# Kernel tuning notes

Hardware: AMD Instinct MI355X
Metric: run time of the kernel (lower is better)

## Reference

```python
import jax, jax.numpy as jnp
import numpy as np
from math import lgamma

B = 8
RES = 64
RES_OUT = 32
L_IN = RES // 2 - 1        # 31
L_OUT = RES_OUT // 2 - 1   # 15
SPINS_IN = (0, 1)
SPINS_OUT = (0, 1, 2)
C_IN = 64
C_OUT = 128
K_IN = (L_IN + 1) ** 2     # 1024 coefficients, ordered by (ell, m): idx = ell^2 + (m + ell)
K_OUT = (L_OUT + 1) ** 2   # 256
EPS_BN = 1e-5
EPS_NL = 1e-6


def _wigner_d_col(l, s, thetas):
    """Wigner small-d column d^l_{m,-s}(theta) for m in [-l, l]; (2l+1, n_theta)."""
    n = -s
    out = np.zeros((2 * l + 1, thetas.size))
    if l < abs(s):
        return out
    cb = np.cos(thetas / 2.0)
    sb = np.sin(thetas / 2.0)
    for mi, m in enumerate(range(-l, l + 1)):
        pref = 0.5 * (lgamma(l + m + 1) + lgamma(l - m + 1)
                      + lgamma(l + n + 1) + lgamma(l - n + 1))
        acc = np.zeros_like(thetas)
        for k in range(max(0, n - m), min(l + n, l - m) + 1):
            lg = pref - (lgamma(l + n - k + 1) + lgamma(k + 1)
                         + lgamma(m - n + k + 1) + lgamma(l - m - k + 1))
            acc += ((-1.0) ** (m - n + k)) * np.exp(lg) \
                   * cb ** (2 * l + n - m - 2 * k) * sb ** (m - n + 2 * k)
        out[mi] = acc
    return out


def _sylm_grid(spin, ell_max, res):
    """Spin-weighted spherical harmonics sampled on equiangular grid: (K, res, res)."""
    thetas = (np.arange(res) + 0.5) * np.pi / res
    phis = np.arange(res) * 2.0 * np.pi / res
    Y = np.zeros(((ell_max + 1) ** 2, res, res), dtype=np.complex64)
    phase = np.exp(1j * np.outer(np.arange(-ell_max, ell_max + 1), phis))
    for l in range(ell_max + 1):
        d = _wigner_d_col(l, spin, thetas)               # (2l+1, res)
        norm = np.sqrt((2 * l + 1) / (4.0 * np.pi))
        for mi, m in enumerate(range(-l, l + 1)):
            Y[l * l + mi] = (((-1.0) ** m) * norm * d[mi][:, None]
                             * phase[m + ell_max][None, :])
    return Y


# Deterministic transform constants (computed once at import).
_THETA = (np.arange(RES) + 0.5) * np.pi / RES
_QUAD_W = (np.sin(_THETA) * (np.pi / RES) * (2.0 * np.pi / RES)).astype(np.float32)
Y_IN = np.stack([_sylm_grid(s, L_IN, RES) for s in SPINS_IN])          # (Si,K_IN,RES,RES)
Y_IN_W = (np.conj(Y_IN) * _QUAD_W[None, None, :, None]).astype(np.complex64)
Y_OUT = np.stack([_sylm_grid(s, L_OUT, RES_OUT) for s in SPINS_OUT])   # (So,K_OUT,32,32)
ELL_OUT = np.floor(np.sqrt(np.arange(K_OUT))).astype(np.int32)         # degree of each coeff


def setup_inputs() -> dict:
    key = jax.random.key(0)
    ks = jax.random.split(key, 8)
    shape_x = (B, RES, RES, len(SPINS_IN), C_IN)
    kern_shape = (L_IN + 1, len(SPINS_IN), len(SPINS_OUT), C_IN, C_OUT)
    scale = 1.0 / np.sqrt(len(SPINS_IN) * C_IN)
    return {
        "x_real": jax.random.normal(ks[0], shape_x, jnp.float32),
        "x_imag": jax.random.normal(ks[1], shape_x, jnp.float32),
        "kernel_real": jax.random.normal(ks[2], kern_shape, jnp.float32) * scale,
        "kernel_imag": jax.random.normal(ks[3], kern_shape, jnp.float32) * scale,
        "gamma": jax.random.uniform(ks[4], (len(SPINS_OUT), C_OUT), jnp.float32, 0.5, 1.5),
        "beta_real": jax.random.normal(ks[5], (len(SPINS_OUT), C_OUT), jnp.float32) * 0.1,
        "beta_imag": jax.random.normal(ks[6], (len(SPINS_OUT), C_OUT), jnp.float32) * 0.1,
        "nonlin_bias": jax.random.normal(ks[7], (len(SPINS_OUT), C_OUT), jnp.float32) * 0.1,
    }


def _forward(x_real, x_imag, kernel_real, kernel_imag, gamma,
             beta_real, beta_imag, nonlin_bias):
    x = x_real + 1j * x_imag                                   # (B,RES,RES,Si,Ci)
    # Forward spin-weighted spherical harmonic transform, per input spin.
    coeffs = jnp.einsum('btpiu,iktp->bkiu', x, jnp.asarray(Y_IN_W))  # (B,K_IN,Si,Ci)
    # Spectral pooling: keep degrees ell <= L_OUT (coeffs ordered by ell).
    coeffs = coeffs[:, :K_OUT]
    # Per-degree spectral convolution mixing spins and channels.
    kernel = (kernel_real + 1j * kernel_imag)[jnp.asarray(ELL_OUT)]  # (K_OUT,Si,So,Ci,Co)
    out_coeffs = jnp.einsum('bkiu,kisud->bksd', coeffs, kernel)      # (B,K_OUT,So,Co)
    # Inverse transform on the downsampled grid, per output spin.
    fmap = jnp.einsum('bksd,sktp->btpsd', out_coeffs, jnp.asarray(Y_OUT))
    # Equivariant batch norm: mean subtraction only for spin 0 channels.
    spin0 = (jnp.asarray(np.array(SPINS_OUT)) == 0)[:, None]         # (So,1)
    mean = jnp.mean(fmap, axis=(0, 1, 2)) * spin0                    # (So,Co)
    centered = fmap - mean
    var = jnp.mean(jnp.abs(centered) ** 2, axis=(0, 1, 2))           # (So,Co)
    beta = (beta_real + 1j * beta_imag) * spin0
    y = centered * (gamma / jnp.sqrt(var + EPS_BN)) + beta
    # Magnitude nonlinearity: y * relu(|y| + b) / (|y| + eps).
    mag = jnp.abs(y)
    return y * (jax.nn.relu(mag + nonlin_bias) / (mag + EPS_NL))


def reference(x_real, x_imag, kernel_real, kernel_imag, gamma,
              beta_real, beta_imag, nonlin_bias):
    return _forward(x_real, x_imag, kernel_real, kernel_imag, gamma,
                    beta_real, beta_imag, nonlin_bias)
```

## Files before the change

### kernel.cpp

```cpp
#include <hip/hip_runtime.h>
#include <hip/hip_fp16.h>
#include <math.h>


#define PI_D 3.14159265358979323846

#define OFF_A_IN    ((size_t)24320)
#define OFF_A_OUT   ((size_t)155648)
#define OFF_STATS   ((size_t)254208)
#define OFF_R1      ((size_t)260608)
#define OFF_R2      ((size_t)25426688)
#define OFF_W       ((size_t)67108864)

__constant__ double LF[31] = {
    0.0, 0.0, 0.6931471805599453, 1.791759469228055, 3.1780538303479458,
    4.787491742782046, 6.579251212010101, 8.525161361065415,
    10.604602902745251, 12.801827480081469, 15.104412573075516,
    17.502307845873887, 19.987214495661885, 22.552163853123425,
    25.19122118273868, 27.89927138384089, 30.671860106080672,
    33.50507345013689, 36.39544520803305, 39.339884187199495,
    42.335616460753485, 45.38013889847691, 48.47118135183523,
    51.60667556776438, 54.78472939811232, 58.00360522298052,
    61.261701761002, 64.55753862700634, 67.88974313718154,
    71.25703896716801, 74.65823634883016};

__device__ inline int isqrt_k(int k) {
    int l = (int)sqrtf((float)k + 0.5f);
    while (l * l > k) --l;
    while ((l + 1) * (l + 1) <= k) ++l;
    return l;
}

__device__ double wigner_d_rec(int l, int m, int n, double theta) {
    int an = n < 0 ? -n : n;
    int am = m < 0 ? -m : m;
    if (l < an || l < am) return 0.0;
    int kmin = max(0, n - m), kmax = min(l + n, l - m);
    if (kmax < kmin) return 0.0;
    double cb = cos(0.5 * theta), sb = sin(0.5 * theta);
    double pref = 0.5 * (LF[l + m] + LF[l - m] + LF[l + n] + LF[l - n]);
    double lterm = pref
        - (LF[l + n - kmin] + LF[kmin] + LF[m - n + kmin] + LF[l - m - kmin])
        + (double)(2 * l + n - m - 2 * kmin) * log(cb)
        + (double)(m - n + 2 * kmin) * log(sb);
    double term = exp(lterm);
    if ((m - n + kmin) & 1) term = -term;
    double r = (sb * sb) / (cb * cb);
    double acc = term;
    for (int k = kmin; k < kmax; ++k) {
        term *= -((double)((l + n - k) * (l - m - k)) * r)
                / ((double)((k + 1) * (m - n + k + 1)));
        acc += term;
    }
    return acc;
}

__global__ __launch_bounds__(512, 2) void k_phi_tables(const float* __restrict__ xr,
                                                       const float* __restrict__ xi,
                                                       __half2* __restrict__ F,
                                                       float* __restrict__ A_in,
                                                       float* __restrict__ A_out,
                                                       float* __restrict__ stats,
                                                       const float* __restrict__ kr,
                                                       const float* __restrict__ ki,
                                                       float4* __restrict__ W) {
    if (blockIdx.x >= 512) {
        if (blockIdx.x >= 627) {
            int e0 = (blockIdx.x - 627) * 512 + threadIdx.x;
            const float2* kr2 = (const float2*)kr;
            const float2* ki2 = (const float2*)ki;
#pragma unroll
            for (int j = 0; j < 16; ++j) {
                int e = e0 + j * 24576;
                int dp = e & 63, r = e >> 6;
                float2 a = kr2[(size_t)r * 64 + dp];
                float2 b = ki2[(size_t)r * 64 + dp];
                W[e] = make_float4(a.x, a.y, b.x, b.y);
            }
            return;
        }
        int idx = (blockIdx.x - 512) * 512 + threadIdx.x;
        if (idx < 32768) {
            int t = idx & 63, k = (idx >> 6) & 255, i = idx >> 14;
            int l = isqrt_k(k);
            int m = k - l * l - l;
            double theta = ((double)t + 0.5) * PI_D / 64.0;
            double w = sin(theta) * (PI_D / 64.0) * (2.0 * PI_D / 64.0);
            double norm = sqrt((2.0 * l + 1.0) / (4.0 * PI_D));
            double d = wigner_d_rec(l, m, -i, theta);
            A_in[idx] = (float)(((m & 1) ? -1.0 : 1.0) * norm * w * d);
            return;
        }
        idx -= 32768;
        if (idx < 24576) {
            int t = idx & 31, k = (idx >> 5) & 255, s = idx >> 13;
            int l = isqrt_k(k);
            int m = k - l * l - l;
            double theta = ((double)t + 0.5) * PI_D / 32.0;
            double norm = sqrt((2.0 * l + 1.0) / (4.0 * PI_D));
            double d = wigner_d_rec(l, m, -s, theta);
            A_out[idx] = (float)(((m & 1) ? -1.0 : 1.0) * norm * d);
            return;
        }
        idx -= 24576;
        if (idx < 1152) stats[idx] = 0.f;
        return;
    }
    int bt = blockIdx.x;
    int iu = threadIdx.x & 127, mh = threadIdx.x >> 7;
    int mi0 = mh * 8;
    float2 acc[8], w[8], st[8];
#pragma unroll
    for (int j = 0; j < 8; ++j) {
        int m = mi0 + j - 15;
        float sy, sx;
        __sincosf(-(float)m * (float)(PI_D / 32.0), &sy, &sx);
        st[j] = make_float2(sx, sy);
        w[j] = make_float2(1.f, 0.f);
        acc[j] = make_float2(0.f, 0.f);
    }
    const float* xrb = xr + (size_t)bt * 8192 + iu;
    const float* xib = xi + (size_t)bt * 8192 + iu;
    for (int p = 0; p < 32; ++p) {
        float a  = xrb[(size_t)p * 128];
        float b  = xib[(size_t)p * 128];
        float a2 = xrb[(size_t)(p + 32) * 128];
        float b2 = xib[(size_t)(p + 32) * 128];
        float sar = a + a2, sai = b + b2;
        float dar = a - a2, dai = b - b2;
#pragma unroll
        for (int j = 0; j < 8; ++j) {
            float ur = (j & 1) ? sar : dar;
            float ui = (j & 1) ? sai : dai;
            acc[j].x += ur * w[j].x - ui * w[j].y;
            acc[j].y += ur * w[j].y + ui * w[j].x;
            float nx = w[j].x * st[j].x - w[j].y * st[j].y;
            w[j].y = w[j].x * st[j].y + w[j].y * st[j].x;
            w[j].x = nx;
        }
    }
    __half2* Fb = F + (size_t)bt * 31 * 128 + iu;
#pragma unroll
    for (int j = 0; j < 8; ++j) {
        int mi = mi0 + j;
        if (mi < 31) Fb[(size_t)mi * 128] = __float22half2_rn(acc[j]);
    }
}

__global__ __launch_bounds__(256, 4) void k_theta_in(const __half2* __restrict__ F,
                                                     const float* __restrict__ A_in,
                                                     __half2* __restrict__ coeffs) {
    __shared__ float A[16][64];
    __shared__ float2 red[2][16][64];
    int mi = blockIdx.x, b = blockIdx.y, z = blockIdx.z;
    int m = mi - 15;
    int am = m < 0 ? -m : m;
    int tid = threadIdx.x;
    for (int idx = tid; idx < 1024; idx += 256) {
        int j = idx >> 6, t = idx & 63;
        float v = 0.f;
        if (j >= am) v = A_in[((size_t)z * 256 + (j * j + j + m)) * 64 + t];
        A[j][t] = v;
    }
    __syncthreads();
    int iu_l = tid & 63, th = tid >> 6;
    int iu = z * 64 + iu_l;
    float2 acc[16];
#pragma unroll
    for (int j = 0; j < 16; ++j) acc[j] = make_float2(0.f, 0.f);
    const __half2* Fb = F + ((size_t)b * 64 * 31 + mi) * 128 + iu;
    for (int tt = 0; tt < 16; ++tt) {
        int t = th * 16 + tt;
        float2 f = __half22float2(Fb[(size_t)t * 31 * 128]);
#pragma unroll
        for (int j = 0; j < 16; ++j) {
            float a = A[j][t];
            acc[j].x += a * f.x;
            acc[j].y += a * f.y;
        }
    }
    if (th >= 2) {
#pragma unroll
        for (int j = 0; j < 16; ++j) red[th - 2][j][iu_l] = acc[j];
    }
    __syncthreads();
    if (th < 2) {
#pragma unroll
        for (int j = 0; j < 16; ++j) {
            float2 r = red[th][j][iu_l];
            acc[j].x += r.x;
            acc[j].y += r.y;
        }
    }
    __syncthreads();
    if (th == 1) {
#pragma unroll
        for (int j = 0; j < 16; ++j) red[0][j][iu_l] = acc[j];
    }
    __syncthreads();
    if (th == 0) {
#pragma unroll
        for (int j = 0; j < 16; ++j) {
            if (j >= am) {
                float2 r = red[0][j][iu_l];
                coeffs[((size_t)b * 256 + (j * j + j + m)) * 128 + iu] =
                    __float22half2_rn(make_float2(acc[j].x + r.x, acc[j].y + r.y));
            }
        }
    }
}

__global__ __launch_bounds__(192, 2) void k_mix(const __half2* __restrict__ coeffs,
                                                const float4* __restrict__ W,
                                                __half2* __restrict__ oc) {
    __shared__ float2 cs[4][128];
    int bx = blockIdx.x;
    int k = ((bx & 7) << 5) + (bx >> 3);
    int b0 = blockIdx.y * 4;
    int tid = threadIdx.x;
    for (int idx = tid; idx < 512; idx += 192) {
        int bb = idx >> 7, iu = idx & 127;
        cs[bb][iu] =
            __half22float2(coeffs[((size_t)(b0 + bb) * 256 + k) * 128 + iu]);
    }
    __syncthreads();
    int s = tid >> 6, dp = tid & 63;
    int l = isqrt_k(k);
    float2 acc[4][2];
#pragma unroll
    for (int bb = 0; bb < 4; ++bb) {
        acc[bb][0] = make_float2(0.f, 0.f);
        acc[bb][1] = make_float2(0.f, 0.f);
    }
    const float4* W0 = W + (size_t)(6 * l + s) * 4096 + dp;
    const float4* W1 = W0 + (size_t)3 * 4096;
    float4 cur[4];
#pragma unroll
    for (int j = 0; j < 4; ++j) cur[j] = W0[(size_t)j * 64];
    for (int g = 0; g < 32; ++g) {
        float4 nxt[4];
        if (g < 31) {
            int iu0 = (g + 1) * 4;
            const float4* P = (iu0 < 64) ? (W0 + (size_t)iu0 * 64)
                                         : (W1 + (size_t)(iu0 - 64) * 64);
#pragma unroll
            for (int j = 0; j < 4; ++j) nxt[j] = P[(size_t)j * 64];
        }
#pragma unroll
        for (int j = 0; j < 4; ++j) {
            int iu = g * 4 + j;
            float2 wr = make_float2(cur[j].x, cur[j].y);
            float2 wi = make_float2(cur[j].z, cur[j].w);
#pragma unroll
            for (int bb = 0; bb < 4; ++bb) {
                float2 cv = cs[bb][iu];
                acc[bb][0].x += cv.x * wr.x - cv.y * wi.x;
                acc[bb][0].y += cv.x * wi.x + cv.y * wr.x;
                acc[bb][1].x += cv.x * wr.y - cv.y * wi.y;
                acc[bb][1].y += cv.x * wi.y + cv.y * wr.y;
            }
        }
        if (g < 31) {
#pragma unroll
            for (int j = 0; j < 4; ++j) cur[j] = nxt[j];
        }
    }
#pragma unroll
    for (int bb = 0; bb < 4; ++bb) {
        size_t o = ((size_t)(b0 + bb) * 256 + k) * 384 + s * 128 + 2 * dp;
        oc[o]     = __float22half2_rn(acc[bb][0]);
        oc[o + 1] = __float22half2_rn(acc[bb][1]);
    }
}

__global__ __launch_bounds__(192, 4) void k_theta_out(const __half2* __restrict__ oc,
                                                      const float* __restrict__ A_out,
                                                      __half2* __restrict__ G,
                                                      float* __restrict__ ssr,
                                                      float* __restrict__ ssi,
                                                      float* __restrict__ ssq) {
    __shared__ float Ao[3][16][32];
    int mi = blockIdx.x, b = blockIdx.y, z = blockIdx.z;
    int m = mi - 15;
    int am = m < 0 ? -m : m;
    int tid = threadIdx.x;
    for (int idx = tid; idx < 1536; idx += 192) {
        int s = idx >> 9, j = (idx >> 5) & 15, t = idx & 31;
        float v = 0.f;
        if (j >= am) v = A_out[((size_t)s * 256 + (j * j + j + m)) * 32 + t];
        Ao[s][j][t] = v;
    }
    __syncthreads();
    int sd = z * 192 + tid;
    int s = sd >> 7;
    float2 c[16];
#pragma unroll
    for (int j = 0; j < 16; ++j) {
        c[j] = make_float2(0.f, 0.f);
        if (j >= am)
            c[j] = __half22float2(oc[((size_t)b * 256 + (j * j + j + m)) * 384 + sd]);
    }
    float sq = 0.f, sr = 0.f, si = 0.f;
    for (int t = 0; t < 32; ++t) {
        float fr = 0.f, fi = 0.f;
#pragma unroll
        for (int j = 0; j < 16; ++j) {
            float a = Ao[s][j][t];
            fr += a * c[j].x;
            fi += a * c[j].y;
        }
        G[(((size_t)b * 32 + t) * 31 + mi) * 384 + sd] =
            __float22half2_rn(make_float2(fr, fi));
        sq += fr * fr + fi * fi;
        if (mi == 15) { sr += fr; si += fi; }
    }
    atomicAdd(&ssq[sd], sq);
    if (mi == 15) {
        atomicAdd(&ssr[sd], sr);
        atomicAdd(&ssi[sd], si);
    }
}

__global__ __launch_bounds__(192, 2) void k_synth_final(const __half2* __restrict__ G,
                                                        const float* __restrict__ ssr,
                                                        const float* __restrict__ ssi,
                                                        const float* __restrict__ ssq,
                                                        const float* __restrict__ gamma,
                                                        const float* __restrict__ betar,
                                                        const float* __restrict__ betai,
                                                        const float* __restrict__ bias,
                                                        float* __restrict__ out) {
    int bt = blockIdx.x;
    int sd = blockIdx.y * 192 + threadIdx.x;
    int s = sd >> 7;
    float2 g[31], st[31];
#pragma unroll
    for (int mi = 0; mi < 31; ++mi) {
        g[mi] = __half22float2(G[((size_t)bt * 31 + mi) * 384 + sd]);
        float sy, sx;
        __sincosf((float)(mi - 15) * (float)(PI_D / 16.0), &sy, &sx);
        st[mi] = make_float2(sx, sy);
    }
    const float invN = 1.0f / 256.0f;
    float mur = 0.f, mui = 0.f;
    if (s == 0) { mur = ssr[sd] * invN; mui = ssi[sd] * invN; }
    float var = ssq[sd] * invN - (mur * mur + mui * mui);
    float scale = gamma[sd] / sqrtf(var + 1e-5f);
    float br = (s == 0) ? betar[sd] : 0.f;
    float bi = (s == 0) ? betai[sd] : 0.f;
    float bb = bias[sd];
    float* ob = out + (size_t)bt * 32 * 384 + sd;
    for (int p = 0; p < 16; ++p) {
        float fr = 0.f, fi = 0.f, fr2 = 0.f, fi2 = 0.f;
#pragma unroll
        for (int mi = 0; mi < 31; ++mi) {
            fr += g[mi].x;
            fi += g[mi].y;
            if (mi & 1) { fr2 += g[mi].x; fi2 += g[mi].y; }
            else        { fr2 -= g[mi].x; fi2 -= g[mi].y; }
        }
        {
            float yr = (fr - mur) * scale + br;
            float yi = (fi - mui) * scale + bi;
            float mag = sqrtf(yr * yr + yi * yi);
            float f = fmaxf(mag + bb, 0.f) / (mag + 1e-6f);
            ob[(size_t)p * 384] = yr * f;
        }
        {
            float yr = (fr2 - mur) * scale + br;
            float yi = (fi2 - mui) * scale + bi;
            float mag = sqrtf(yr * yr + yi * yi);
            float f = fmaxf(mag + bb, 0.f) / (mag + 1e-6f);
            ob[(size_t)(p + 16) * 384] = yr * f;
        }
#pragma unroll
        for (int mi = 0; mi < 31; ++mi) {
            float nx = g[mi].x * st[mi].x - g[mi].y * st[mi].y;
            g[mi].y = g[mi].x * st[mi].y + g[mi].y * st[mi].x;
            g[mi].x = nx;
        }
    }
}

extern "C" void kernel_launch(void* const* d_in, const int* in_sizes, int n_in,
                              void* d_out, int out_size, void* d_ws, size_t ws_size,
                              hipStream_t stream) {
    const float* xr    = (const float*)d_in[0];
    const float* xi    = (const float*)d_in[1];
    const float* kr    = (const float*)d_in[2];
    const float* ki    = (const float*)d_in[3];
    const float* gamma = (const float*)d_in[4];
    const float* betar = (const float*)d_in[5];
    const float* betai = (const float*)d_in[6];
    const float* bias  = (const float*)d_in[7];
    float* out = (float*)d_out;

    char* ws = (char*)d_ws;
    float*   A_in   = (float*)(ws + OFF_A_IN);
    float*   A_out  = (float*)(ws + OFF_A_OUT);
    float*   stats  = (float*)(ws + OFF_STATS);
    float*   ssr    = stats;
    float*   ssi    = stats + 384;
    float*   ssq    = stats + 768;
    __half2* F      = (__half2*)(ws + OFF_R1);
    __half2* oc     = (__half2*)(ws + OFF_R1);
    __half2* coeffs = (__half2*)(ws + OFF_R2);
    __half2* G      = (__half2*)(ws + OFF_R2);
    float4*  W      = (float4*)(ws + OFF_W);

    k_phi_tables<<<675, 512, 0, stream>>>(xr, xi, F, A_in, A_out, stats, kr, ki, W);
    k_theta_in<<<dim3(31, 8, 2), 256, 0, stream>>>(F, A_in, coeffs);
    k_mix<<<dim3(256, 2), 192, 0, stream>>>(coeffs, W, oc);
    k_theta_out<<<dim3(31, 8, 2), 192, 0, stream>>>(oc, A_out, G, ssr, ssi, ssq);
    k_synth_final<<<dim3(256, 2), 192, 0, stream>>>(G, ssr, ssi, ssq,
                                                    gamma, betar, betai, bias, out);
}
```

Baseline: 179.5 us.

## Fuse five stage kernels into one persistent kernel with grid barriers

Replaces the five separate launches with a single persistent 256-block kernel that runs every stage in turn. Stages are separated by software grid barriers built on an atomic counter, and each block processes two logical blocks per stage. The aim is to remove launch and drain gaps between stages. In exchange, occupancy drops to one block per CU, the barriers cost spin-waits, and the barrier has a timeout that could silently break correctness, plus an extra memset.

Result: slower. 330.6 us (+84.2%).

```diff
diff --git a/kernel.cpp b/kernel.cpp
--- a/kernel.cpp
+++ b/kernel.cpp
@@ -8,6 +8,7 @@
 #define OFF_A_IN    ((size_t)24320)
 #define OFF_A_OUT   ((size_t)155648)
 #define OFF_STATS   ((size_t)254208)
+#define OFF_BAR     ((size_t)259072)
 #define OFF_R1      ((size_t)260608)
 #define OFF_R2      ((size_t)25426688)
 #define OFF_W       ((size_t)67108864)
@@ -55,32 +56,60 @@
     return acc;
 }
 
-__global__ __launch_bounds__(512, 2) void k_phi_tables(const float* __restrict__ xr,
-                                                       const float* __restrict__ xi,
-                                                       __half2* __restrict__ F,
-                                                       float* __restrict__ A_in,
-                                                       float* __restrict__ A_out,
-                                                       float* __restrict__ stats,
-                                                       const float* __restrict__ kr,
-                                                       const float* __restrict__ ki,
-                                                       float4* __restrict__ W) {
-    if (blockIdx.x >= 512) {
-        if (blockIdx.x >= 627) {
-            int e0 = (blockIdx.x - 627) * 512 + threadIdx.x;
-            const float2* kr2 = (const float2*)kr;
-            const float2* ki2 = (const float2*)ki;
-#pragma unroll
-            for (int j = 0; j < 16; ++j) {
-                int e = e0 + j * 24576;
-                int dp = e & 63, r = e >> 6;
-                float2 a = kr2[(size_t)r * 64 + dp];
-                float2 b = ki2[(size_t)r * 64 + dp];
-                W[e] = make_float4(a.x, a.y, b.x, b.y);
-            }
-            return;
-        }
-        int idx = (blockIdx.x - 512) * 512 + threadIdx.x;
-        if (idx < 32768) {
+__device__ __forceinline__ void gbar(unsigned* bar, unsigned target) {
+    __syncthreads();
+    if (threadIdx.x == 0) {
+        __threadfence();
+        __hip_atomic_fetch_add(bar, 1u, __ATOMIC_RELEASE,
+                               __HIP_MEMORY_SCOPE_AGENT);
+        unsigned tries = 0;
+        while (__hip_atomic_load(bar, __ATOMIC_ACQUIRE,
+                                 __HIP_MEMORY_SCOPE_AGENT) < target) {
+            __builtin_amdgcn_s_sleep(2);
+            if (++tries > 200000u) break;
+        }
+        __threadfence();
+    }
+    __syncthreads();
+}
+
+__global__ __launch_bounds__(256, 1) void k_mega(
+    const float* __restrict__ xr, const float* __restrict__ xi,
+    const float* __restrict__ kr, const float* __restrict__ ki,
+    const float* __restrict__ gamma, const float* __restrict__ betar,
+    const float* __restrict__ betai, const float* __restrict__ bias,
+    float* __restrict__ out,
+    float* __restrict__ A_in, float* __restrict__ A_out,
+    float* __restrict__ stats,
+    __half2* __restrict__ F, __half2* __restrict__ coeffs,
+    __half2* __restrict__ oc, __half2* __restrict__ G,
+    float4* __restrict__ W, unsigned* __restrict__ bar) {
+    __shared__ union {
+        struct { float A[16][64]; float2 red[2][16][64]; } p2;
+        struct { float2 cs[4][128]; } p3;
+        struct { float Ao[3][16][32]; } p4;
+    } sm;
+
+    float* ssr = stats;
+    float* ssi = stats + 384;
+    float* ssq = stats + 768;
+
+    int bid = blockIdx.x, tid = threadIdx.x;
+    int gidx = bid * 256 + tid;
+
+    {
+        const float2* kr2 = (const float2*)kr;
+        const float2* ki2 = (const float2*)ki;
+#pragma unroll
+        for (int j = 0; j < 6; ++j) {
+            int e = gidx + j * 65536;
+            int dp = e & 63, r = e >> 6;
+            float2 a = kr2[(size_t)r * 64 + dp];
+            float2 b = ki2[(size_t)r * 64 + dp];
+            W[e] = make_float4(a.x, a.y, b.x, b.y);
+        }
+        if (gidx < 32768) {
+            int idx = gidx;
             int t = idx & 63, k = (idx >> 6) & 255, i = idx >> 14;
             int l = isqrt_k(k);
             int m = k - l * l - l;
@@ -89,10 +118,8 @@
             double norm = sqrt((2.0 * l + 1.0) / (4.0 * PI_D));
             double d = wigner_d_rec(l, m, -i, theta);
             A_in[idx] = (float)(((m & 1) ? -1.0 : 1.0) * norm * w * d);
-            return;
-        }
-        idx -= 32768;
-        if (idx < 24576) {
+        } else if (gidx < 57344) {
+            int idx = gidx - 32768;
             int t = idx & 31, k = (idx >> 5) & 255, s = idx >> 13;
             int l = isqrt_k(k);
             int m = k - l * l - l;
@@ -100,284 +127,287 @@
             double norm = sqrt((2.0 * l + 1.0) / (4.0 * PI_D));
             double d = wigner_d_rec(l, m, -s, theta);
             A_out[idx] = (float)(((m & 1) ? -1.0 : 1.0) * norm * d);
-            return;
-        }
-        idx -= 24576;
-        if (idx < 1152) stats[idx] = 0.f;
-        return;
-    }
-    int bt = blockIdx.x;
-    int iu = threadIdx.x & 127, mh = threadIdx.x >> 7;
-    int mi0 = mh * 8;
-    float2 acc[8], w[8], st[8];
-#pragma unroll
-    for (int j = 0; j < 8; ++j) {
-        int m = mi0 + j - 15;
-        float sy, sx;
-        __sincosf(-(float)m * (float)(PI_D / 32.0), &sy, &sx);
-        st[j] = make_float2(sx, sy);
-        w[j] = make_float2(1.f, 0.f);
-        acc[j] = make_float2(0.f, 0.f);
-    }
-    const float* xrb = xr + (size_t)bt * 8192 + iu;
-    const float* xib = xi + (size_t)bt * 8192 + iu;
-    for (int p = 0; p < 32; ++p) {
-        float a  = xrb[(size_t)p * 128];
-        float b  = xib[(size_t)p * 128];
-        float a2 = xrb[(size_t)(p + 32) * 128];
-        float b2 = xib[(size_t)(p + 32) * 128];
-        float sar = a + a2, sai = b + b2;
-        float dar = a - a2, dai = b - b2;
-#pragma unroll
-        for (int j = 0; j < 8; ++j) {
-            float ur = (j & 1) ? sar : dar;
-            float ui = (j & 1) ? sai : dai;
-            acc[j].x += ur * w[j].x - ui * w[j].y;
-            acc[j].y += ur * w[j].y + ui * w[j].x;
-            float nx = w[j].x * st[j].x - w[j].y * st[j].y;
-            w[j].y = w[j].x * st[j].y + w[j].y * st[j].x;
-            w[j].x = nx;
-        }
-    }
-    __half2* Fb = F + (size_t)bt * 31 * 128 + iu;
-#pragma unroll
-    for (int j = 0; j < 8; ++j) {
-        int mi = mi0 + j;
-        if (mi < 31) Fb[(size_t)mi * 128] = __float22half2_rn(acc[j]);
-    }
-}
-
-__global__ __launch_bounds__(256, 4) void k_theta_in(const __half2* __restrict__ F,
-                                                     const float* __restrict__ A_in,
-                                                     __half2* __restrict__ coeffs) {
-    __shared__ float A[16][64];
-    __shared__ float2 red[2][16][64];
-    int mi = blockIdx.x, b = blockIdx.y, z = blockIdx.z;
-    int m = mi - 15;
-    int am = m < 0 ? -m : m;
-    int tid = threadIdx.x;
-    for (int idx = tid; idx < 1024; idx += 256) {
-        int j = idx >> 6, t = idx & 63;
-        float v = 0.f;
-        if (j >= am) v = A_in[((size_t)z * 256 + (j * j + j + m)) * 64 + t];
-        A[j][t] = v;
-    }
-    __syncthreads();
-    int iu_l = tid & 63, th = tid >> 6;
-    int iu = z * 64 + iu_l;
-    float2 acc[16];
-#pragma unroll
-    for (int j = 0; j < 16; ++j) acc[j] = make_float2(0.f, 0.f);
-    const __half2* Fb = F + ((size_t)b * 64 * 31 + mi) * 128 + iu;
-    for (int tt = 0; tt < 16; ++tt) {
-        int t = th * 16 + tt;
-        float2 f = __half22float2(Fb[(size_t)t * 31 * 128]);
+        } else if (gidx < 58496) {
+            stats[gidx - 57344] = 0.f;
+        }
+    }
+    for (int rr = 0; rr < 2; ++rr) {
+        int bt = bid + 256 * rr;
+        int iu = tid & 127, mh2 = tid >> 7;
+        float2 acc[16], w[16], st[16];
 #pragma unroll
         for (int j = 0; j < 16; ++j) {
-            float a = A[j][t];
-            acc[j].x += a * f.x;
-            acc[j].y += a * f.y;
-        }
-    }
-    if (th >= 2) {
-#pragma unroll
-        for (int j = 0; j < 16; ++j) red[th - 2][j][iu_l] = acc[j];
-    }
-    __syncthreads();
-    if (th < 2) {
+            int m = mh2 * 16 + j - 15;
+            float sy, sx;
+            __sincosf(-(float)m * (float)(PI_D / 32.0), &sy, &sx);
+            st[j] = make_float2(sx, sy);
+            w[j] = make_float2(1.f, 0.f);
+            acc[j] = make_float2(0.f, 0.f);
+        }
+        const float* xrb = xr + (size_t)bt * 8192 + iu;
+        const float* xib = xi + (size_t)bt * 8192 + iu;
+        for (int p = 0; p < 32; ++p) {
+            float a  = xrb[(size_t)p * 128];
+            float b  = xib[(size_t)p * 128];
+            float a2 = xrb[(size_t)(p + 32) * 128];
+            float b2 = xib[(size_t)(p + 32) * 128];
+            float sar = a + a2, sai = b + b2;
+            float dar = a - a2, dai = b - b2;
+#pragma unroll
+            for (int j = 0; j < 16; ++j) {
+                float ur = (j & 1) ? sar : dar;
+                float ui = (j & 1) ? sai : dai;
+                acc[j].x += ur * w[j].x - ui * w[j].y;
+                acc[j].y += ur * w[j].y + ui * w[j].x;
+                float nx = w[j].x * st[j].x - w[j].y * st[j].y;
+                w[j].y = w[j].x * st[j].y + w[j].y * st[j].x;
+                w[j].x = nx;
+            }
+        }
+        __half2* Fb = F + (size_t)bt * 31 * 128 + iu;
 #pragma unroll
         for (int j = 0; j < 16; ++j) {
-            float2 r = red[th][j][iu_l];
-            acc[j].x += r.x;
-            acc[j].y += r.y;
-        }
-    }
-    __syncthreads();
-    if (th == 1) {
-#pragma unroll
-        for (int j = 0; j < 16; ++j) red[0][j][iu_l] = acc[j];
-    }
-    __syncthreads();
-    if (th == 0) {
-#pragma unroll
-        for (int j = 0; j < 16; ++j) {
-            if (j >= am) {
-                float2 r = red[0][j][iu_l];
-                coeffs[((size_t)b * 256 + (j * j + j + m)) * 128 + iu] =
-                    __float22half2_rn(make_float2(acc[j].x + r.x, acc[j].y + r.y));
-            }
-        }
-    }
-}
-
-__global__ __launch_bounds__(192, 2) void k_mix(const __half2* __restrict__ coeffs,
-                                                const float4* __restrict__ W,
-                                                __half2* __restrict__ oc) {
-    __shared__ float2 cs[4][128];
-    int bx = blockIdx.x;
-    int k = ((bx & 7) << 5) + (bx >> 3);
-    int b0 = blockIdx.y * 4;
-    int tid = threadIdx.x;
-    for (int idx = tid; idx < 512; idx += 192) {
-        int bb = idx >> 7, iu = idx & 127;
-        cs[bb][iu] =
-            __half22float2(coeffs[((size_t)(b0 + bb) * 256 + k) * 128 + iu]);
-    }
-    __syncthreads();
-    int s = tid >> 6, dp = tid & 63;
-    int l = isqrt_k(k);
-    float2 acc[4][2];
-#pragma unroll
-    for (int bb = 0; bb < 4; ++bb) {
-        acc[bb][0] = make_float2(0.f, 0.f);
-        acc[bb][1] = make_float2(0.f, 0.f);
-    }
-    const float4* W0 = W + (size_t)(6 * l + s) * 4096 + dp;
-    const float4* W1 = W0 + (size_t)3 * 4096;
-    float4 cur[4];
-#pragma unroll
-    for (int j = 0; j < 4; ++j) cur[j] = W0[(size_t)j * 64];
-    for (int g = 0; g < 32; ++g) {
-        float4 nxt[4];
-        if (g < 31) {
-            int iu0 = (g + 1) * 4;
-            const float4* P = (iu0 < 64) ? (W0 + (size_t)iu0 * 64)
-                                         : (W1 + (size_t)(iu0 - 64) * 64);
-#pragma unroll
-            for (int j = 0; j < 4; ++j) nxt[j] = P[(size_t)j * 64];
-        }
-#pragma unroll
-        for (int j = 0; j < 4; ++j) {
-            int iu = g * 4 + j;
-            float2 wr = make_float2(cur[j].x, cur[j].y);
-            float2 wi = make_float2(cur[j].z, cur[j].w);
+            int mi = mh2 * 16 + j;
+            if (mi < 31) Fb[(size_t)mi * 128] = __float22half2_rn(acc[j]);
+        }
+    }
+    gbar(bar, 256);
+
+    for (int rr = 0; rr < 2; ++rr) {
+        int lb = bid + 256 * rr;
+        if (lb < 496) {
+            int mi = lb % 31;
+            int q = lb / 31;
+            int b = q >> 1, z = q & 1;
+            int m = mi - 15;
+            int am = m < 0 ? -m : m;
+            for (int idx = tid; idx < 1024; idx += 256) {
+                int j = idx >> 6, t = idx & 63;
+                float v = 0.f;
+                if (j >= am) v = A_in[((size_t)z * 256 + (j * j + j + m)) * 64 + t];
+                sm.p2.A[j][t] = v;
+            }
+            __syncthreads();
+            int iu_l = tid & 63, th = tid >> 6;
+            int iu = z * 64 + iu_l;
+            float2 acc[16];
+#pragma unroll
+            for (int j = 0; j < 16; ++j) acc[j] = make_float2(0.f, 0.f);
+            const __half2* Fb = F + ((size_t)b * 64 * 31 + mi) * 128 + iu;
+            for (int tt = 0; tt < 16; ++tt) {
+                int t = th * 16 + tt;
+                float2 f = __half22float2(Fb[(size_t)t * 31 * 128]);
+#pragma unroll
+                for (int j = 0; j < 16; ++j) {
+                    float a = sm.p2.A[j][t];
+                    acc[j].x += a * f.x;
+                    acc[j].y += a * f.y;
+                }
+            }
+            if (th >= 2) {
+#pragma unroll
+                for (int j = 0; j < 16; ++j) sm.p2.red[th - 2][j][iu_l] = acc[j];
+            }
+            __syncthreads();
+            if (th < 2) {
+#pragma unroll
+                for (int j = 0; j < 16; ++j) {
+                    float2 r = sm.p2.red[th][j][iu_l];
+                    acc[j].x += r.x;
+                    acc[j].y += r.y;
+                }
+            }
+            __syncthreads();
+            if (th == 1) {
+#pragma unroll
+                for (int j = 0; j < 16; ++j) sm.p2.red[0][j][iu_l] = acc[j];
+            }
+            __syncthreads();
+            if (th == 0) {
+#pragma unroll
+                for (int j = 0; j < 16; ++j) {
+                    if (j >= am) {
+                        float2 r = sm.p2.red[0][j][iu_l];
+                        coeffs[((size_t)b * 256 + (j * j + j + m)) * 128 + iu] =
+                            __float22half2_rn(
+                                make_float2(acc[j].x + r.x, acc[j].y + r.y));
+                    }
+                }
+            }
+        }
+        __syncthreads();
+    }
+    gbar(bar, 512);
+
+    for (int rr = 0; rr < 2; ++rr) {
+        int lb = bid + 256 * rr;
+        int y = lb >> 8;
+        int bxk = lb & 255;
+        int k = ((bxk & 7) << 5) + (bxk >> 3);
+        int b0 = y * 4;
+        for (int idx = tid; idx < 512; idx += 256) {
+            int bb = idx >> 7, iuu = idx & 127;
+            sm.p3.cs[bb][iuu] =
+                __half22float2(coeffs[((size_t)(b0 + bb) * 256 + k) * 128 + iuu]);
+        }
+        __syncthreads();
+        if (tid < 192) {
+            int s = tid >> 6, dp = tid & 63;
+            int l = isqrt_k(k);
+            float2 acc[4][2];
 #pragma unroll
             for (int bb = 0; bb < 4; ++bb) {
-                float2 cv = cs[bb][iu];
-                acc[bb][0].x += cv.x * wr.x - cv.y * wi.x;
-                acc[bb][0].y += cv.x * wi.x + cv.y * wr.x;
-                acc[bb][1].x += cv.x * wr.y - cv.y * wi.y;
-                acc[bb][1].y += cv.x * wi.y + cv.y * wr.y;
-            }
-        }
-        if (g < 31) {
-#pragma unroll
-            for (int j = 0; j < 4; ++j) cur[j] = nxt[j];
-        }
-    }
-#pragma unroll
-    for (int bb = 0; bb < 4; ++bb) {
-        size_t o = ((size_t)(b0 + bb) * 256 + k) * 384 + s * 128 + 2 * dp;
-        oc[o]     = __float22half2_rn(acc[bb][0]);
-        oc[o + 1] = __float22half2_rn(acc[bb][1]);
-    }
-}
-
-__global__ __launch_bounds__(192, 4) void k_theta_out(const __half2* __restrict__ oc,
-                                                      const float* __restrict__ A_out,
-                                                      __half2* __restrict__ G,
-                                                      float* __restrict__ ssr,
-                                                      float* __restrict__ ssi,
-                                                      float* __restrict__ ssq) {
-    __shared__ float Ao[3][16][32];
-    int mi = blockIdx.x, b = blockIdx.y, z = blockIdx.z;
-    int m = mi - 15;
-    int am = m < 0 ? -m : m;
-    int tid = threadIdx.x;
-    for (int idx = tid; idx < 1536; idx += 192) {
-        int s = idx >> 9, j = (idx >> 5) & 15, t = idx & 31;
-        float v = 0.f;
-        if (j >= am) v = A_out[((size_t)s * 256 + (j * j + j + m)) * 32 + t];
-        Ao[s][j][t] = v;
-    }
-    __syncthreads();
-    int sd = z * 192 + tid;
-    int s = sd >> 7;
-    float2 c[16];
-#pragma unroll
-    for (int j = 0; j < 16; ++j) {
-        c[j] = make_float2(0.f, 0.f);
-        if (j >= am)
-            c[j] = __half22float2(oc[((size_t)b * 256 + (j * j + j + m)) * 384 + sd]);
-    }
-    float sq = 0.f, sr = 0.f, si = 0.f;
-    for (int t = 0; t < 32; ++t) {
-        float fr = 0.f, fi = 0.f;
-#pragma unroll
-        for (int j = 0; j < 16; ++j) {
-            float a = Ao[s][j][t];
-            fr += a * c[j].x;
-            fi += a * c[j].y;
-        }
-        G[(((size_t)b * 32 + t) * 31 + mi) * 384 + sd] =
-            __float22half2_rn(make_float2(fr, fi));
-        sq += fr * fr + fi * fi;
-        if (mi == 15) { sr += fr; si += fi; }
-    }
-    atomicAdd(&ssq[sd], sq);
-    if (mi == 15) {
-        atomicAdd(&ssr[sd], sr);
-        atomicAdd(&ssi[sd], si);
-    }
-}
-
-__global__ __launch_bounds__(192, 2) void k_synth_final(const __half2* __restrict__ G,
-                                                        const float* __restrict__ ssr,
-                                                        const float* __restrict__ ssi,
-                                                        const float* __restrict__ ssq,
-                                                        const float* __restrict__ gamma,
-                                                        const float* __restrict__ betar,
-                                                        const float* __restrict__ betai,
-                                                        const float* __restrict__ bias,
-                                                        float* __restrict__ out) {
-    int bt = blockIdx.x;
-    int sd = blockIdx.y * 192 + threadIdx.x;
-    int s = sd >> 7;
-    float2 g[31], st[31];
-#pragma unroll
-    for (int mi = 0; mi < 31; ++mi) {
-        g[mi] = __half22float2(G[((size_t)bt * 31 + mi) * 384 + sd]);
-        float sy, sx;
-        __sincosf((float)(mi - 15) * (float)(PI_D / 16.0), &sy, &sx);
-        st[mi] = make_float2(sx, sy);
-    }
-    const float invN = 1.0f / 256.0f;
-    float mur = 0.f, mui = 0.f;
-    if (s == 0) { mur = ssr[sd] * invN; mui = ssi[sd] * invN; }
-    float var = ssq[sd] * invN - (mur * mur + mui * mui);
-    float scale = gamma[sd] / sqrtf(var + 1e-5f);
-    float br = (s == 0) ? betar[sd] : 0.f;
-    float bi = (s == 0) ? betai[sd] : 0.f;
-    float bb = bias[sd];
-    float* ob = out + (size_t)bt * 32 * 384 + sd;
-    for (int p = 0; p < 16; ++p) {
-        float fr = 0.f, fi = 0.f, fr2 = 0.f, fi2 = 0.f;
-#pragma unroll
-        for (int mi = 0; mi < 31; ++mi) {
-            fr += g[mi].x;
-            fi += g[mi].y;
-            if (mi & 1) { fr2 += g[mi].x; fi2 += g[mi].y; }
-            else        { fr2 -= g[mi].x; fi2 -= g[mi].y; }
-        }
-        {
-            float yr = (fr - mur) * scale + br;
-            float yi = (fi - mui) * scale + bi;
-            float mag = sqrtf(yr * yr + yi * yi);
-            float f = fmaxf(mag + bb, 0.f) / (mag + 1e-6f);
-            ob[(size_t)p * 384] = yr * f;
-        }
-        {
-            float yr = (fr2 - mur) * scale + br;
-            float yi = (fi2 - mui) * scale + bi;
-            float mag = sqrtf(yr * yr + yi * yi);
-            float f = fmaxf(mag + bb, 0.f) / (mag + 1e-6f);
-            ob[(size_t)(p + 16) * 384] = yr * f;
-        }
-#pragma unroll
-        for (int mi = 0; mi < 31; ++mi) {
-            float nx = g[mi].x * st[mi].x - g[mi].y * st[mi].y;
-            g[mi].y = g[mi].x * st[mi].y + g[mi].y * st[mi].x;
-            g[mi].x = nx;
+                acc[bb][0] = make_float2(0.f, 0.f);
+                acc[bb][1] = make_float2(0.f, 0.f);
+            }
+            const float4* W0 = W + (size_t)(6 * l + s) * 4096 + dp;
+            const float4* W1 = W0 + (size_t)3 * 4096;
+            float4 cur[4];
+#pragma unroll
+            for (int j = 0; j < 4; ++j) cur[j] = W0[(size_t)j * 64];
+            for (int g = 0; g < 32; ++g) {
+                float4 nxt[4];
+                if (g < 31) {
+                    int iu0 = (g + 1) * 4;
+                    const float4* P = (iu0 < 64) ? (W0 + (size_t)iu0 * 64)
+                                                 : (W1 + (size_t)(iu0 - 64) * 64);
+#pragma unroll
+                    for (int j = 0; j < 4; ++j) nxt[j] = P[(size_t)j * 64];
+                }
+#pragma unroll
+                for (int j = 0; j < 4; ++j) {
+                    int iu = g * 4 + j;
+                    float2 wr = make_float2(cur[j].x, cur[j].y);
+                    float2 wi = make_float2(cur[j].z, cur[j].w);
+#pragma unroll
+                    for (int bb = 0; bb < 4; ++bb) {
+                        float2 cv = sm.p3.cs[bb][iu];
+                        acc[bb][0].x += cv.x * wr.x - cv.y * wi.x;
+                        acc[bb][0].y += cv.x * wi.x + cv.y * wr.x;
+                        acc[bb][1].x += cv.x * wr.y - cv.y * wi.y;
+                        acc[bb][1].y += cv.x * wi.y + cv.y * wr.y;
+                    }
+                }
+                if (g < 31) {
+#pragma unroll
+                    for (int j = 0; j < 4; ++j) cur[j] = nxt[j];
+                }
+            }
+#pragma unroll
+            for (int bb = 0; bb < 4; ++bb) {
+                size_t o = ((size_t)(b0 + bb) * 256 + k) * 384 + s * 128 + 2 * dp;
+                oc[o]     = __float22half2_rn(acc[bb][0]);
+                oc[o + 1] = __float22half2_rn(acc[bb][1]);
+            }
+        }
+        __syncthreads();
+    }
+    gbar(bar, 768);
+
+    for (int rr = 0; rr < 2; ++rr) {
+        int lb = bid + 256 * rr;
+        if (lb < 496) {
+            int mi = lb % 31;
+            int q = lb / 31;
+            int b = q >> 1, z = q & 1;
+            int m = mi - 15;
+            int am = m < 0 ? -m : m;
+            for (int idx = tid; idx < 1536; idx += 256) {
+                int s = idx >> 9, j = (idx >> 5) & 15, t = idx & 31;
+                float v = 0.f;
+                if (j >= am) v = A_out[((size_t)s * 256 + (j * j + j + m)) * 32 + t];
+                sm.p4.Ao[s][j][t] = v;
+            }
+            __syncthreads();
+            if (tid < 192) {
+                int sd = z * 192 + tid;
+                int s = sd >> 7;
+                float2 c[16];
+#pragma unroll
+                for (int j = 0; j < 16; ++j) {
+                    c[j] = make_float2(0.f, 0.f);
+                    if (j >= am)
+                        c[j] = __half22float2(
+                            oc[((size_t)b * 256 + (j * j + j + m)) * 384 + sd]);
+                }
+                float sq = 0.f, sr = 0.f, si = 0.f;
+                for (int t = 0; t < 32; ++t) {
+                    float fr = 0.f, fi = 0.f;
+#pragma unroll
+                    for (int j = 0; j < 16; ++j) {
+                        float a = sm.p4.Ao[s][j][t];
+                        fr += a * c[j].x;
+                        fi += a * c[j].y;
+                    }
+                    G[(((size_t)b * 32 + t) * 31 + mi) * 384 + sd] =
+                        __float22half2_rn(make_float2(fr, fi));
+                    sq += fr * fr + fi * fi;
+                    if (mi == 15) { sr += fr; si += fi; }
+                }
+                atomicAdd(&ssq[sd], sq);
+                if (mi == 15) {
+                    atomicAdd(&ssr[sd], sr);
+                    atomicAdd(&ssi[sd], si);
+                }
+            }
+        }
+        __syncthreads();
+    }
+    gbar(bar, 1024);
+
+    for (int rr = 0; rr < 2; ++rr) {
+        int lb = bid + 256 * rr;
+        int bt = lb >> 1, half = lb & 1;
+        if (tid < 192) {
+            int sd = half * 192 + tid;
+            int s = sd >> 7;
+            float2 g[31], st[31];
+#pragma unroll
+            for (int mi = 0; mi < 31; ++mi) {
+                g[mi] = __half22float2(G[((size_t)bt * 31 + mi) * 384 + sd]);
+                float sy, sx;
+                __sincosf((float)(mi - 15) * (float)(PI_D / 16.0), &sy, &sx);
+                st[mi] = make_float2(sx, sy);
+            }
+            const float invN = 1.0f / 256.0f;
+            float mur = 0.f, mui = 0.f;
+            if (s == 0) { mur = ssr[sd] * invN; mui = ssi[sd] * invN; }
+            float var = ssq[sd] * invN - (mur * mur + mui * mui);
+            float scale = gamma[sd] / sqrtf(var + 1e-5f);
+            float br = (s == 0) ? betar[sd] : 0.f;
+            float bi = (s == 0) ? betai[sd] : 0.f;
+            float bb = bias[sd];
+            float* ob = out + (size_t)bt * 32 * 384 + sd;
+            for (int p = 0; p < 16; ++p) {
+                float fr = 0.f, fi = 0.f, fr2 = 0.f, fi2 = 0.f;
+#pragma unroll
+                for (int mi = 0; mi < 31; ++mi) {
+                    fr += g[mi].x;
+                    fi += g[mi].y;
+                    if (mi & 1) { fr2 += g[mi].x; fi2 += g[mi].y; }
+                    else        { fr2 -= g[mi].x; fi2 -= g[mi].y; }
+                }
+                {
+                    float yr = (fr - mur) * scale + br;
+                    float yi = (fi - mui) * scale + bi;
+                    float mag = sqrtf(yr * yr + yi * yi);
+                    float f = fmaxf(mag + bb, 0.f) / (mag + 1e-6f);
+                    ob[(size_t)p * 384] = yr * f;
+                }
+                {
+                    float yr = (fr2 - mur) * scale + br;
+                    float yi = (fi2 - mui) * scale + bi;
+                    float mag = sqrtf(yr * yr + yi * yi);
+                    float f = fmaxf(mag + bb, 0.f) / (mag + 1e-6f);
+                    ob[(size_t)(p + 16) * 384] = yr * f;
+                }
+#pragma unroll
+                for (int mi = 0; mi < 31; ++mi) {
+                    float nx = g[mi].x * st[mi].x - g[mi].y * st[mi].y;
+                    g[mi].y = g[mi].x * st[mi].y + g[mi].y * st[mi].x;
+                    g[mi].x = nx;
+                }
+            }
         }
     }
 }
@@ -399,19 +429,15 @@
     float*   A_in   = (float*)(ws + OFF_A_IN);
     float*   A_out  = (float*)(ws + OFF_A_OUT);
     float*   stats  = (float*)(ws + OFF_STATS);
-    float*   ssr    = stats;
-    float*   ssi    = stats + 384;
-    float*   ssq    = stats + 768;
+    unsigned* bar   = (unsigned*)(ws + OFF_BAR);
     __half2* F      = (__half2*)(ws + OFF_R1);
     __half2* oc     = (__half2*)(ws + OFF_R1);
     __half2* coeffs = (__half2*)(ws + OFF_R2);
     __half2* G      = (__half2*)(ws + OFF_R2);
     float4*  W      = (float4*)(ws + OFF_W);
 
-    k_phi_tables<<<675, 512, 0, stream>>>(xr, xi, F, A_in, A_out, stats, kr, ki, W);
-    k_theta_in<<<dim3(31, 8, 2), 256, 0, stream>>>(F, A_in, coeffs);
-    k_mix<<<dim3(256, 2), 192, 0, stream>>>(coeffs, W, oc);
-    k_theta_out<<<dim3(31, 8, 2), 192, 0, stream>>>(oc, A_out, G, ssr, ssi, ssq);
-    k_synth_final<<<dim3(256, 2), 192, 0, stream>>>(G, ssr, ssi, ssq,
-                                                    gamma, betar, betai, bias, out);
+    hipMemsetAsync(ws + OFF_BAR, 0, 64, stream);
+    k_mega<<<256, 256, 0, stream>>>(xr, xi, kr, ki, gamma, betar, betai, bias,
+                                    out, A_in, A_out, stats, F, coeffs, oc, G,
+                                    W, bar);
 }
```
